# Optimization experiments

Measured on AMD Instinct MI355X. Metric: run time of the kernel, lower is better.

## Reference

```python
import jax, jax.numpy as jnp
import numpy as np

B, L = 2048, 8192
IN, H, OUT = 128, 512, 10
N_FRAMES = L // IN  # frame_step == frame_size -> non-overlapping unfold == reshape


def _lstm_layer(xs, W_ih, W_hh, b):
    """xs: [T, B, D_in]; returns (hs [T, B, H], h_T [B, H]).
    PyTorch gate order: i, f, g, o."""
    Bsz = xs.shape[1]
    h0 = jnp.zeros((Bsz, H), xs.dtype)
    c0 = jnp.zeros((Bsz, H), xs.dtype)

    def step(carry, x_t):
        h, c = carry
        gates = x_t @ W_ih.T + h @ W_hh.T + b  # [B, 4H]
        i, f, g, o = jnp.split(gates, 4, axis=-1)
        c = jax.nn.sigmoid(f) * c + jax.nn.sigmoid(i) * jnp.tanh(g)
        h = jax.nn.sigmoid(o) * jnp.tanh(c)
        return (h, c), h

    (hT, _), hs = jax.lax.scan(step, (h0, c0), xs)
    return hs, hT


def setup_inputs() -> dict:
    key = jax.random.key(0)
    ks = jax.random.split(key, 12)
    s_in = 1.0 / np.sqrt(H)
    return {
        "xb": jax.random.normal(ks[0], (B, L), jnp.float32),
        "W_ih0": jax.random.normal(ks[1], (4 * H, IN), jnp.float32) * s_in,
        "W_hh0": jax.random.normal(ks[2], (4 * H, H), jnp.float32) * s_in,
        "b0": jax.random.normal(ks[3], (4 * H,), jnp.float32) * s_in,
        "W_ih1": jax.random.normal(ks[4], (4 * H, H), jnp.float32) * s_in,
        "W_hh1": jax.random.normal(ks[5], (4 * H, H), jnp.float32) * s_in,
        "b1": jax.random.normal(ks[6], (4 * H,), jnp.float32) * s_in,
        "W_out": jax.random.normal(ks[7], (OUT, H), jnp.float32) * s_in,
        "b_out": jax.random.normal(ks[8], (OUT,), jnp.float32) * s_in,
    }


def reference(xb, W_ih0, W_hh0, b0, W_ih1, W_hh1, b1, W_out, b_out):
    # unfold(1, fs, fs) with step==size -> reshape; transpose to time-major
    frames = xb.reshape(B, N_FRAMES, IN).transpose(1, 0, 2)  # [T, B, IN]
    hs0, _ = _lstm_layer(frames, W_ih0, W_hh0, b0)           # [T, B, H]
    _, hT1 = _lstm_layer(hs0, W_ih1, W_hh1, b1)              # [B, H]
    return hT1 @ W_out.T + b_out                             # [B, OUT]
```

## Files before the change

### kernel.cpp

```cpp
#include <hip/hip_runtime.h>
#include <hip/hip_bf16.h>


typedef _Float16 f16x8 __attribute__((ext_vector_type(8)));
typedef float f32x4 __attribute__((ext_vector_type(4)));

#define Bsz 2048
#define Lsz 8192
#define Tsz 64

__global__ void cvt_f32_f16(const float* __restrict__ src, _Float16* __restrict__ dst, int n4) {
    int stride = gridDim.x * blockDim.x;
    for (int i = blockIdx.x * blockDim.x + threadIdx.x; i < n4; i += stride) {
        float4 v = ((const float4*)src)[i];
        union { _Float16 h[4]; ushort4 u; } o;
        o.h[0] = (_Float16)v.x; o.h[1] = (_Float16)v.y;
        o.h[2] = (_Float16)v.z; o.h[3] = (_Float16)v.w;
        ((ushort4*)dst)[i] = o.u;
    }
}

__global__ void pack_w(const float* __restrict__ Wih, const float* __restrict__ Whh,
                       _Float16* __restrict__ dst, int K1) {
    int KT = K1 + 512;
    int n4 = 2048 * KT / 4;
    int stride = gridDim.x * blockDim.x;
    for (int i = blockIdx.x * blockDim.x + threadIdx.x; i < n4; i += stride) {
        int row = i / (KT / 4);
        int col = (i % (KT / 4)) * 4;
        const float* s = (col < K1) ? (Wih + (size_t)row * K1 + col)
                                    : (Whh + (size_t)row * 512 + (col - K1));
        float4 v = *(const float4*)s;
        union { _Float16 h[4]; ushort4 u; } o;
        o.h[0] = (_Float16)v.x; o.h[1] = (_Float16)v.y;
        o.h[2] = (_Float16)v.z; o.h[3] = (_Float16)v.w;
        ((ushort4*)dst)[i] = o.u;
    }
}

__device__ __forceinline__ float fsig(float x)  { return 1.0f / (1.0f + __expf(-x)); }
__device__ __forceinline__ float ftanh(float x) { return 1.0f - 2.0f / (__expf(2.0f * x) + 1.0f); }

template<int K1>
__device__ __forceinline__ void stage_v6(
    const _Float16* __restrict__ A1, int lda1,
    const _Float16* __restrict__ A2,
    const _Float16* __restrict__ Wcat,
    int hcb, int rowtile, int k0, char* buf, int tid)
{
    constexpr int KT = K1 + 512;
    const int wv = tid >> 6;
#pragma unroll
    for (int q = 0; q < 2; ++q) {
        const int j  = q * 64 + (tid >> 3);
        const int cg = (((tid & 7) ^ (j & 7)) << 3);
        const int wrow = ((j >> 5) << 9) + hcb * 32 + (j & 31);
        const _Float16* src = Wcat + (size_t)wrow * KT + k0 + cg;
        __builtin_amdgcn_global_load_lds(
            (const __attribute__((address_space(1))) void*)src,
            (__attribute__((address_space(3))) void*)(buf + q * 8192 + wv * 1024),
            16, 0, 0);
    }
#pragma unroll
    for (int q = 0; q < 4; ++q) {
        const int row  = q * 64 + (tid >> 3);
        const int cg   = (((tid & 7) ^ (row & 7)) << 3);
        const int kcol = k0 + cg;
        const int brow = rowtile * 256 + row;
        const _Float16* src = (kcol < K1)
            ? (A1 + (size_t)brow * lda1 + kcol)
            : (A2 + (size_t)brow * 512 + (kcol - K1));
        __builtin_amdgcn_global_load_lds(
            (const __attribute__((address_space(1))) void*)src,
            (__attribute__((address_space(3))) void*)(buf + 16384 + q * 8192 + wv * 1024),
            16, 0, 0);
    }
}

template<int K1>
__device__ __forceinline__ void step_v6(
    const _Float16* __restrict__ A1, int lda1,
    const _Float16* __restrict__ A2,
    const _Float16* __restrict__ Wcat,
    const float* __restrict__ bias,
    float* __restrict__ c,
    _Float16* __restrict__ h_out,
    int rowtile, int hcb, char* lds)
{
    constexpr int KT  = K1 + 512;
    constexpr int NIT = KT / 64;
    const int tid = threadIdx.x;
    const int ln  = tid & 63;
    const int wv  = tid >> 6;
    const int llo = ln & 15, lhi = ln >> 4;
    const int wr  = wv >> 1, wc = wv & 1;

    f32x4 acc[4][4] = {};

    stage_v6<K1>(A1, lda1, A2, Wcat, hcb, rowtile, 0, lds, tid);
    __syncthreads();

    for (int it = 0; it < NIT; ++it) {
        char* cur = lds + (it & 1) * 49152;
        if (it + 1 < NIT)
            stage_v6<K1>(A1, lda1, A2, Wcat, hcb, rowtile, (it + 1) * 64,
                         lds + ((it + 1) & 1) * 49152, tid);
#pragma unroll
        for (int ks = 0; ks < 2; ++ks) {
            const int gsw = (((ks * 4 + lhi) ^ (llo & 7)) << 4);
            f16x8 a[4], b[4];
#pragma unroll
            for (int mi = 0; mi < 4; ++mi)
                a[mi] = *(const f16x8*)(cur + 16384 + (wr * 64 + mi * 16 + llo) * 128 + gsw);
#pragma unroll
            for (int cf = 0; cf < 4; ++cf)
                b[cf] = *(const f16x8*)(cur + (wc * 64 + cf * 16 + llo) * 128 + gsw);
#pragma unroll
            for (int mi = 0; mi < 4; ++mi)
#pragma unroll
                for (int cf = 0; cf < 4; ++cf)
                    acc[mi][cf] = __builtin_amdgcn_mfma_f32_16x16x32_f16(
                        a[mi], b[cf], acc[mi][cf], 0, 0, 0);
        }
        __syncthreads();
    }

    float* gl = (float*)lds;
#pragma unroll
    for (int mi = 0; mi < 4; ++mi)
#pragma unroll
        for (int cf = 0; cf < 4; ++cf) {
            const int col = wc * 64 + cf * 16 + llo;
#pragma unroll
            for (int r = 0; r < 4; ++r) {
                const int row = wr * 64 + mi * 16 + lhi * 4 + r;
                gl[row * 128 + col] = acc[mi][cf][r];
            }
        }
    __syncthreads();

    const int lc   = tid & 31;
    const int ro   = tid >> 5;
    const int hcol = hcb * 32 + lc;
    float bz[4];
#pragma unroll
    for (int g = 0; g < 4; ++g) bz[g] = bias[g * 512 + hcol];
#pragma unroll
    for (int i = 0; i < 16; ++i) {
        const int row = i * 16 + ro;
        float iv = gl[row * 128 +  0 + lc] + bz[0];
        float fv = gl[row * 128 + 32 + lc] + bz[1];
        float gv = gl[row * 128 + 64 + lc] + bz[2];
        float ov = gl[row * 128 + 96 + lc] + bz[3];
        const size_t idx = (size_t)(rowtile * 256 + row) * 512 + hcol;
        float co = c[idx];
        float cn = fsig(fv) * co + fsig(iv) * ftanh(gv);
        float hn = fsig(ov) * ftanh(cn);
        c[idx] = cn;
        h_out[idx] = (_Float16)hn;
    }
}

__global__ __launch_bounds__(512, 2) void lstm_round(
    int t0, int t1,
    const _Float16* __restrict__ xb16,
    const _Float16* __restrict__ Wc0, const float* __restrict__ b0, float* __restrict__ c0,
    _Float16* __restrict__ h00, _Float16* __restrict__ h01,
    const _Float16* __restrict__ Wc1, const float* __restrict__ b1, float* __restrict__ c1,
    _Float16* __restrict__ h10, _Float16* __restrict__ h11)
{
    __shared__ __align__(16) char lds[131072];
    const int bid     = blockIdx.x;
    const int x       = bid & 7;
    const int q       = bid >> 3;
    const int layer   = q >> 4;
    const int rowtile = (q >> 1) & 7;
    const int hcb     = x * 2 + (q & 1);

    if (layer == 0) {
        if (t0 < 0) return;
        const _Float16* hr = (t0 & 1) ? h01 : h00;
        _Float16*       hw = (t0 & 1) ? h00 : h01;
        step_v6<128>(xb16 + (size_t)t0 * 128, Lsz, hr, Wc0, b0, c0, hw, rowtile, hcb, lds);
    } else {
        if (t1 < 0) return;
        const _Float16* h0in = ((t1 + 1) & 1) ? h01 : h00;
        const _Float16* hr   = (t1 & 1) ? h11 : h10;
        _Float16*       hw   = (t1 & 1) ? h10 : h11;
        step_v6<512>(h0in, 512, hr, Wc1, b1, c1, hw, rowtile, hcb, lds);
    }
}

__global__ void proj_kernel(const _Float16* __restrict__ h1,
                            const float* __restrict__ Wout,
                            const float* __restrict__ bout,
                            float* __restrict__ out)
{
    int tid = blockIdx.x * blockDim.x + threadIdx.x;
    if (tid >= Bsz * 10) return;
    int b = tid / 10, o = tid % 10;
    float s = bout[o];
    const _Float16* hrow = h1 + (size_t)b * 512;
    const float* wrow = Wout + (size_t)o * 512;
    for (int k = 0; k < 512; ++k) s += (float)hrow[k] * wrow[k];
    out[tid] = s;
}

extern "C" void kernel_launch(void* const* d_in, const int* in_sizes, int n_in,
                              void* d_out, int out_size, void* d_ws, size_t ws_size,
                              hipStream_t stream) {
    const float* xb    = (const float*)d_in[0];
    const float* W_ih0 = (const float*)d_in[1];
    const float* W_hh0 = (const float*)d_in[2];
    const float* b0    = (const float*)d_in[3];
    const float* W_ih1 = (const float*)d_in[4];
    const float* W_hh1 = (const float*)d_in[5];
    const float* b1    = (const float*)d_in[6];
    const float* W_out = (const float*)d_in[7];
    const float* b_out = (const float*)d_in[8];
    float* out = (float*)d_out;

    char* ws = (char*)d_ws;
    size_t off = 0;
    auto alloc = [&](size_t bytes) -> void* {
        void* p = ws + off;
        off += (bytes + 255) & ~(size_t)255;
        return p;
    };
    _Float16* xb16 = (_Float16*)alloc((size_t)Bsz * Lsz * 2);
    _Float16* Wc0  = (_Float16*)alloc((size_t)2048 * 640 * 2);
    _Float16* Wc1  = (_Float16*)alloc((size_t)2048 * 1024 * 2);
    _Float16* h00  = (_Float16*)alloc((size_t)Bsz * 512 * 2);
    _Float16* h01  = (_Float16*)alloc((size_t)Bsz * 512 * 2);
    _Float16* h10  = (_Float16*)alloc((size_t)Bsz * 512 * 2);
    _Float16* h11  = (_Float16*)alloc((size_t)Bsz * 512 * 2);
    float* c0 = (float*)alloc((size_t)Bsz * 512 * 4);
    float* c1 = (float*)alloc((size_t)Bsz * 512 * 4);

    cvt_f32_f16<<<2048, 256, 0, stream>>>(xb, xb16, Bsz * Lsz / 4);
    pack_w<<<1280, 256, 0, stream>>>(W_ih0, W_hh0, Wc0, 128);
    pack_w<<<2048, 256, 0, stream>>>(W_ih1, W_hh1, Wc1, 512);

    hipMemsetAsync(h00, 0, (size_t)Bsz * 512 * 2, stream);
    hipMemsetAsync(h10, 0, (size_t)Bsz * 512 * 2, stream);
    hipMemsetAsync(c0, 0, (size_t)Bsz * 512 * 4, stream);
    hipMemsetAsync(c1, 0, (size_t)Bsz * 512 * 4, stream);

    for (int r = 0; r <= Tsz; ++r) {
        int t0 = (r < Tsz) ? r : -1;
        int t1 = r - 1;
        lstm_round<<<dim3(256), 512, 0, stream>>>(t0, t1,
            xb16, Wc0, b0, c0, h00, h01,
            Wc1, b1, c1, h10, h11);
    }

    proj_kernel<<<(Bsz * 10 + 255) / 256, 256, 0, stream>>>(h10, W_out, b_out, out);
}
```

Baseline: 1.668 ms.

## Replace per-step launches with persistent kernel using a global atomic grid barrier

```diff
diff --git a/kernel.cpp b/kernel.cpp
--- a/kernel.cpp
+++ b/kernel.cpp
@@ -8,6 +8,7 @@
 #define Bsz 2048
 #define Lsz 8192
 #define Tsz 64
+#define NBLK 256
 
 __global__ void cvt_f32_f16(const float* __restrict__ src, _Float16* __restrict__ dst, int n4) {
     int stride = gridDim.x * blockDim.x;
@@ -41,8 +42,15 @@
 __device__ __forceinline__ float fsig(float x)  { return 1.0f / (1.0f + __expf(-x)); }
 __device__ __forceinline__ float ftanh(float x) { return 1.0f - 2.0f / (__expf(2.0f * x) + 1.0f); }
 
-template<int K1>
-__device__ __forceinline__ void stage_v6(
+template<int AUX>
+__device__ __forceinline__ void gll16(const _Float16* src, char* dst) {
+    __builtin_amdgcn_global_load_lds(
+        (const __attribute__((address_space(1))) void*)src,
+        (__attribute__((address_space(3))) void*)dst, 16, 0, AUX);
+}
+
+template<int K1, int AUX1>
+__device__ __forceinline__ void stage_v7(
     const _Float16* __restrict__ A1, int lda1,
     const _Float16* __restrict__ A2,
     const _Float16* __restrict__ Wcat,
@@ -51,34 +59,25 @@
     constexpr int KT = K1 + 512;
     const int wv = tid >> 6;
 #pragma unroll
-    for (int q = 0; q < 2; ++q) {
-        const int j  = q * 64 + (tid >> 3);
+    for (int qq = 0; qq < 4; ++qq) {
+        const int j  = qq * 64 + (tid >> 3);
         const int cg = (((tid & 7) ^ (j & 7)) << 3);
-        const int wrow = ((j >> 5) << 9) + hcb * 32 + (j & 31);
-        const _Float16* src = Wcat + (size_t)wrow * KT + k0 + cg;
-        __builtin_amdgcn_global_load_lds(
-            (const __attribute__((address_space(1))) void*)src,
-            (__attribute__((address_space(3))) void*)(buf + q * 8192 + wv * 1024),
-            16, 0, 0);
-    }
-#pragma unroll
-    for (int q = 0; q < 4; ++q) {
-        const int row  = q * 64 + (tid >> 3);
+        const int wrow = ((j >> 6) << 9) + hcb * 64 + (j & 63);
+        gll16<0>(Wcat + (size_t)wrow * KT + k0 + cg, buf + qq * 8192 + wv * 1024);
+    }
+#pragma unroll
+    for (int qq = 0; qq < 2; ++qq) {
+        const int row  = qq * 64 + (tid >> 3);
         const int cg   = (((tid & 7) ^ (row & 7)) << 3);
-        const int kcol = k0 + cg;
-        const int brow = rowtile * 256 + row;
-        const _Float16* src = (kcol < K1)
-            ? (A1 + (size_t)brow * lda1 + kcol)
-            : (A2 + (size_t)brow * 512 + (kcol - K1));
-        __builtin_amdgcn_global_load_lds(
-            (const __attribute__((address_space(1))) void*)src,
-            (__attribute__((address_space(3))) void*)(buf + 16384 + q * 8192 + wv * 1024),
-            16, 0, 0);
-    }
-}
-
-template<int K1>
-__device__ __forceinline__ void step_v6(
+        const int brow = rowtile * 128 + row;
+        char* d = buf + 32768 + qq * 8192 + wv * 1024;
+        if (k0 < K1) gll16<AUX1>(A1 + (size_t)brow * lda1 + k0 + cg, d);
+        else         gll16<16>(A2 + (size_t)brow * 512 + (k0 - K1) + cg, d);
+    }
+}
+
+template<int K1, int AUX1>
+__device__ __forceinline__ void step_v7(
     const _Float16* __restrict__ A1, int lda1,
     const _Float16* __restrict__ A2,
     const _Float16* __restrict__ Wcat,
@@ -93,25 +92,26 @@
     const int ln  = tid & 63;
     const int wv  = tid >> 6;
     const int llo = ln & 15, lhi = ln >> 4;
-    const int wr  = wv >> 1, wc = wv & 1;
+    const int wr  = wv >> 2, wc = wv & 3;
 
     f32x4 acc[4][4] = {};
 
-    stage_v6<K1>(A1, lda1, A2, Wcat, hcb, rowtile, 0, lds, tid);
+    stage_v7<K1, AUX1>(A1, lda1, A2, Wcat, hcb, rowtile, 0, lds, tid);
     __syncthreads();
 
+#pragma unroll 2
     for (int it = 0; it < NIT; ++it) {
         char* cur = lds + (it & 1) * 49152;
         if (it + 1 < NIT)
-            stage_v6<K1>(A1, lda1, A2, Wcat, hcb, rowtile, (it + 1) * 64,
-                         lds + ((it + 1) & 1) * 49152, tid);
+            stage_v7<K1, AUX1>(A1, lda1, A2, Wcat, hcb, rowtile, (it + 1) * 64,
+                               lds + ((it + 1) & 1) * 49152, tid);
 #pragma unroll
         for (int ks = 0; ks < 2; ++ks) {
             const int gsw = (((ks * 4 + lhi) ^ (llo & 7)) << 4);
             f16x8 a[4], b[4];
 #pragma unroll
             for (int mi = 0; mi < 4; ++mi)
-                a[mi] = *(const f16x8*)(cur + 16384 + (wr * 64 + mi * 16 + llo) * 128 + gsw);
+                a[mi] = *(const f16x8*)(cur + 32768 + (wr * 64 + mi * 16 + llo) * 128 + gsw);
 #pragma unroll
             for (int cf = 0; cf < 4; ++cf)
                 b[cf] = *(const f16x8*)(cur + (wc * 64 + cf * 16 + llo) * 128 + gsw);
@@ -132,62 +132,88 @@
         for (int cf = 0; cf < 4; ++cf) {
             const int col = wc * 64 + cf * 16 + llo;
 #pragma unroll
-            for (int r = 0; r < 4; ++r) {
-                const int row = wr * 64 + mi * 16 + lhi * 4 + r;
-                gl[row * 128 + col] = acc[mi][cf][r];
+            for (int rr = 0; rr < 4; ++rr) {
+                const int row = wr * 64 + mi * 16 + lhi * 4 + rr;
+                gl[row * 256 + col] = acc[mi][cf][rr];
             }
         }
     __syncthreads();
 
-    const int lc   = tid & 31;
+    const int lc2  = (tid & 31) << 1;
     const int ro   = tid >> 5;
-    const int hcol = hcb * 32 + lc;
-    float bz[4];
-#pragma unroll
-    for (int g = 0; g < 4; ++g) bz[g] = bias[g * 512 + hcol];
-#pragma unroll
-    for (int i = 0; i < 16; ++i) {
+    const int hcol = hcb * 64 + lc2;
+    const float bi0 = bias[hcol],        bi1 = bias[hcol + 1];
+    const float bf0 = bias[512 + hcol],  bf1 = bias[512 + hcol + 1];
+    const float bg0 = bias[1024 + hcol], bg1 = bias[1024 + hcol + 1];
+    const float bo0 = bias[1536 + hcol], bo1 = bias[1536 + hcol + 1];
+#pragma unroll
+    for (int i = 0; i < 8; ++i) {
         const int row = i * 16 + ro;
-        float iv = gl[row * 128 +  0 + lc] + bz[0];
-        float fv = gl[row * 128 + 32 + lc] + bz[1];
-        float gv = gl[row * 128 + 64 + lc] + bz[2];
-        float ov = gl[row * 128 + 96 + lc] + bz[3];
-        const size_t idx = (size_t)(rowtile * 256 + row) * 512 + hcol;
-        float co = c[idx];
-        float cn = fsig(fv) * co + fsig(iv) * ftanh(gv);
-        float hn = fsig(ov) * ftanh(cn);
-        c[idx] = cn;
-        h_out[idx] = (_Float16)hn;
-    }
-}
-
-__global__ __launch_bounds__(512, 2) void lstm_round(
-    int t0, int t1,
+        const float* g0 = gl + row * 256 + lc2;
+        float iv0 = g0[0]   + bi0, iv1 = g0[1]   + bi1;
+        float fv0 = g0[64]  + bf0, fv1 = g0[65]  + bf1;
+        float gv0 = g0[128] + bg0, gv1 = g0[129] + bg1;
+        float ov0 = g0[192] + bo0, ov1 = g0[193] + bo1;
+        const size_t base = (size_t)(rowtile * 128 + row) * 512 + hcol;
+        float2 cc = *(const float2*)&c[base];
+        float cn0 = fsig(fv0) * cc.x + fsig(iv0) * ftanh(gv0);
+        float cn1 = fsig(fv1) * cc.y + fsig(iv1) * ftanh(gv1);
+        float hn0 = fsig(ov0) * ftanh(cn0);
+        float hn1 = fsig(ov1) * ftanh(cn1);
+        float2 cw; cw.x = cn0; cw.y = cn1;
+        *(float2*)&c[base] = cw;
+        union { _Float16 h2[2]; unsigned u; } hp;
+        hp.h2[0] = (_Float16)hn0; hp.h2[1] = (_Float16)hn1;
+        __hip_atomic_store((unsigned*)(h_out + base), hp.u,
+                           __ATOMIC_RELAXED, __HIP_MEMORY_SCOPE_AGENT);
+    }
+}
+
+__global__ __launch_bounds__(512, 1) void lstm_persist(
     const _Float16* __restrict__ xb16,
     const _Float16* __restrict__ Wc0, const float* __restrict__ b0, float* __restrict__ c0,
     _Float16* __restrict__ h00, _Float16* __restrict__ h01,
     const _Float16* __restrict__ Wc1, const float* __restrict__ b1, float* __restrict__ c1,
-    _Float16* __restrict__ h10, _Float16* __restrict__ h11)
+    _Float16* __restrict__ h10, _Float16* __restrict__ h11,
+    unsigned* __restrict__ cnt)
 {
     __shared__ __align__(16) char lds[131072];
     const int bid     = blockIdx.x;
     const int x       = bid & 7;
     const int q       = bid >> 3;
-    const int layer   = q >> 4;
-    const int rowtile = (q >> 1) & 7;
-    const int hcb     = x * 2 + (q & 1);
-
-    if (layer == 0) {
-        if (t0 < 0) return;
-        const _Float16* hr = (t0 & 1) ? h01 : h00;
-        _Float16*       hw = (t0 & 1) ? h00 : h01;
-        step_v6<128>(xb16 + (size_t)t0 * 128, Lsz, hr, Wc0, b0, c0, hw, rowtile, hcb, lds);
-    } else {
-        if (t1 < 0) return;
-        const _Float16* h0in = ((t1 + 1) & 1) ? h01 : h00;
-        const _Float16* hr   = (t1 & 1) ? h11 : h10;
-        _Float16*       hw   = (t1 & 1) ? h10 : h11;
-        step_v6<512>(h0in, 512, hr, Wc1, b1, c1, hw, rowtile, hcb, lds);
+    const int layer   = q & 1;
+    const int rowtile = q >> 1;
+    const int hcb     = x;
+
+    for (int r = 0; r <= Tsz; ++r) {
+        if (layer == 0) {
+            if (r < Tsz) {
+                const int t0 = r;
+                const _Float16* hr = (t0 & 1) ? h01 : h00;
+                _Float16*       hw = (t0 & 1) ? h00 : h01;
+                step_v7<128, 0>(xb16 + (size_t)t0 * 128, Lsz, hr, Wc0, b0, c0, hw,
+                                rowtile, hcb, lds);
+            }
+        } else {
+            if (r >= 1) {
+                const int t1 = r - 1;
+                const _Float16* h0in = ((t1 + 1) & 1) ? h01 : h00;
+                const _Float16* hr   = (t1 & 1) ? h11 : h10;
+                _Float16*       hw   = (t1 & 1) ? h10 : h11;
+                step_v7<512, 16>(h0in, 512, hr, Wc1, b1, c1, hw, rowtile, hcb, lds);
+            }
+        }
+        if (r < Tsz) {
+            __syncthreads();
+            if (threadIdx.x == 0) {
+                __hip_atomic_fetch_add(cnt, 1u, __ATOMIC_RELAXED, __HIP_MEMORY_SCOPE_AGENT);
+                const unsigned target = (unsigned)NBLK * (r + 1);
+                while (__hip_atomic_load(cnt, __ATOMIC_RELAXED, __HIP_MEMORY_SCOPE_AGENT) < target)
+                    __builtin_amdgcn_s_sleep(1);
+            }
+            __syncthreads();
+            __builtin_amdgcn_sched_barrier(0);
+        }
     }
 }
 
@@ -236,6 +262,7 @@
     _Float16* h11  = (_Float16*)alloc((size_t)Bsz * 512 * 2);
     float* c0 = (float*)alloc((size_t)Bsz * 512 * 4);
     float* c1 = (float*)alloc((size_t)Bsz * 512 * 4);
+    unsigned* cnt = (unsigned*)alloc(256);
 
     cvt_f32_f16<<<2048, 256, 0, stream>>>(xb, xb16, Bsz * Lsz / 4);
     pack_w<<<1280, 256, 0, stream>>>(W_ih0, W_hh0, Wc0, 128);
@@ -245,14 +272,10 @@
     hipMemsetAsync(h10, 0, (size_t)Bsz * 512 * 2, stream);
     hipMemsetAsync(c0, 0, (size_t)Bsz * 512 * 4, stream);
     hipMemsetAsync(c1, 0, (size_t)Bsz * 512 * 4, stream);
-
-    for (int r = 0; r <= Tsz; ++r) {
-        int t0 = (r < Tsz) ? r : -1;
-        int t1 = r - 1;
-        lstm_round<<<dim3(256), 512, 0, stream>>>(t0, t1,
-            xb16, Wc0, b0, c0, h00, h01,
-            Wc1, b1, c1, h10, h11);
-    }
+    hipMemsetAsync(cnt, 0, 256, stream);
+
+    lstm_persist<<<dim3(NBLK), 512, 0, stream>>>(
+        xb16, Wc0, b0, c0, h00, h01, Wc1, b1, c1, h10, h11, cnt);
 
     proj_kernel<<<(Bsz * 10 + 255) / 256, 256, 0, stream>>>(h10, W_out, b_out, out);
 }
```

Result: slower. 1.914 ms (+14.8%).
